# Kernel tuning notes

Measured on AMD Instinct MI355X. Metric: run time of the kernel, lower is better.

Reference implementation:

```python
import jax, jax.numpy as jnp
import numpy as np


def setup_inputs() -> dict:
    key = jax.random.key(0)
    k1, k2, k3, k4, k5 = jax.random.split(key, 5)
    B, T, H = 32, 4096, 256
    D = 2 * H  # encoder feature dim
    hidden = jax.random.normal(k1, (B, D), dtype=jnp.float32)
    encoder_outputs = jax.random.normal(k2, (B, T, D), dtype=jnp.float32)
    # torch nn.Linear(4H, H): weight [H, 4H], bias [H]
    W_attn = jax.random.normal(k3, (H, 4 * H), dtype=jnp.float32) * (1.0 / np.sqrt(4 * H))
    b_attn = jax.random.normal(k4, (H,), dtype=jnp.float32) * 0.01
    v = jax.random.uniform(k5, (H,), dtype=jnp.float32)  # torch.rand init
    return {"hidden": hidden, "encoder_outputs": encoder_outputs,
            "W_attn": W_attn, "b_attn": b_attn, "v": v}


def reference(hidden, encoder_outputs, W_attn, b_attn, v):
    D = hidden.shape[-1]  # 2*H
    # Split Linear(4H->H) weight into the hidden part and encoder part so we
    # never materialize the [B,T,4H] concat: cat(h,e) @ W.T == h @ Wh.T + e @ We.T
    W_h = W_attn[:, :D]   # [H, 2H]
    W_e = W_attn[:, D:]   # [H, 2H]
    h_proj = hidden @ W_h.T                     # [B, H]
    e_proj = jnp.einsum('btd,hd->bth', encoder_outputs, W_e)  # [B, T, H]
    energy = jnp.tanh(h_proj[:, None, :] + e_proj + b_attn)   # [B, T, H]
    scores = energy @ v                          # [B, T]
    attn_weights = jax.nn.softmax(scores, axis=1)  # softmax over timesteps
    context = jnp.einsum('bt,btd->bd', attn_weights, encoder_outputs)  # [B, 2H]
    return context, attn_weights
```

## Files before the change

kernel.cpp:

```cpp
#include <hip/hip_runtime.h>
#include <hip/hip_bf16.h>
#include <math.h>

#define B_  32
#define T_  4096
#define H_  256
#define D_  512

#define WS_PRE    0
#define WS_WEHI   32768
#define WS_P      294912
#define WS_ML     819200
#define WS_PCTX   827392

using short8  = __attribute__((ext_vector_type(8))) short;
using float4v = __attribute__((ext_vector_type(4))) float;

__device__ __forceinline__ unsigned cvt2_bf16(float lo, float hi) {
    union { __hip_bfloat162 h; unsigned u; } cv;
    cv.h = __float22bfloat162_rn(make_float2(lo, hi));
    return cv.u;
}
__device__ __forceinline__ short8 cvt8_bf16(const float* a) {
    union { unsigned u[4]; short8 s; } r;
    r.u[0] = cvt2_bf16(a[0], a[1]);
    r.u[1] = cvt2_bf16(a[2], a[3]);
    r.u[2] = cvt2_bf16(a[4], a[5]);
    r.u[3] = cvt2_bf16(a[6], a[7]);
    return r.s;
}

__device__ __forceinline__ float fast_tanh(float x) {
    float e = __expf(2.0f * x);
    return 1.0f - 2.0f * __builtin_amdgcn_rcpf(e + 1.0f);
}

__global__ __launch_bounds__(256)
void prep_kernel(const float* __restrict__ hidden,
                 const float* __restrict__ W_attn,
                 const float* __restrict__ b_attn,
                 unsigned char* __restrict__ ws) {
    int blk = blockIdx.x;
    int tid = threadIdx.x;
    if (blk < 32) {
        int b = blk, h = tid;
        const float4* hv = (const float4*)(hidden + b * D_);
        const float4* wv = (const float4*)(W_attn + (size_t)h * 1024);
        float s = 0.f;
        #pragma unroll 4
        for (int d4 = 0; d4 < D_ / 4; ++d4) {
            float4 a = hv[d4], w = wv[d4];
            s += a.x * w.x + a.y * w.y + a.z * w.z + a.w * w.w;
        }
        ((float*)(ws + WS_PRE))[b * H_ + h] = s + b_attn[h];
    } else {
        int q = (blk - 32) * 256 + tid;
        unsigned short* whi = (unsigned short*)(ws + WS_WEHI);
        #pragma unroll
        for (int i = 0; i < 4; ++i) {
            int idx4 = q + i * 8192;
            int n = idx4 >> 7, k = (idx4 & 127) << 2;
            int t = k >> 5, kin = k & 31;
            int quad = kin >> 3, e = kin & 7;
            int slot = quad ^ ((n >> 1) & 3);
            float4 w = *(const float4*)(W_attn + (size_t)n * 1024 + 512 + k);
            unsigned lo = cvt2_bf16(w.x, w.y);
            unsigned hi = cvt2_bf16(w.z, w.w);
            unsigned short* dst = whi + t * 8192 + n * 32 + slot * 8 + e;
            *(uint2*)dst = make_uint2(lo, hi);
        }
    }
}

#define BM 128
#define BN 256
#define BK 32
#define LDT 40
#define KIT 16

__global__ __launch_bounds__(512, 4)
void gemm_scores_kernel(const float* __restrict__ enc,
                        unsigned char* __restrict__ ws,
                        const float* __restrict__ v) {
    __shared__ unsigned short sA[2][BM * LDT];
    __shared__ float sScoreP[4][BM];
    __shared__ float sP[BM];
    __shared__ float sRed[4];

    const float*          pre = (const float*)(ws + WS_PRE);
    const unsigned short* weh = (const unsigned short*)(ws + WS_WEHI);

    int tid = threadIdx.x;
    int m0  = blockIdx.x * BM;
    int b   = m0 >> 12;

    int rowA = tid & 127, cgA = tid >> 7;
    const float* gA = enc + (size_t)(m0 + rowA) * D_ + cgA * 8;

    int wave = tid >> 6, lane = tid & 63;
    int wm = wave & 1, wn = wave >> 1;
    int quad = lane >> 4, l16 = lane & 15;

    int slotB = quad ^ ((l16 >> 1) & 3);
    const unsigned short* bBase = weh + (wn * 64 + l16) * 32 + slotB * 8;

    float4v acc[4][4] = {};

    float aX[8], aY[8];
    short8 bhA[4], bhB[4];

    {
        const float4* p0 = (const float4*)gA;
        float4 x0 = p0[0], x1 = p0[1];
        #pragma unroll
        for (int j = 0; j < 4; ++j)
            bhA[j] = *(const short8*)(bBase + j * 512);
        const float4* p1 = (const float4*)(gA + BK);
        float4 y0 = p1[0], y1 = p1[1];
        #pragma unroll
        for (int j = 0; j < 4; ++j)
            bhB[j] = *(const short8*)(bBase + 8192 + j * 512);

        float tmp[8];
        *(float4*)tmp = x0; *(float4*)(tmp + 4) = x1;
        *(short8*)&sA[0][rowA * LDT + cgA * 8] = cvt8_bf16(tmp);
        *(float4*)aY = y0; *(float4*)(aY + 4) = y1;
    }
    __builtin_amdgcn_s_waitcnt(0xc07f);
    __builtin_amdgcn_s_barrier();

#define K_STEP(kk, CUR, NXT, Acons, Aload, Bcur, Bnxt)                        \
    {                                                                         \
        if ((kk) + 1 < KIT) {                                                 \
            const unsigned short* pb = bBase + ((kk) + 1) * 8192;             \
            Bnxt[0] = *(const short8*)(pb);                                   \
            Bnxt[1] = *(const short8*)(pb + 512);                             \
            Bnxt[2] = *(const short8*)(pb + 1024);                            \
            Bnxt[3] = *(const short8*)(pb + 1536);                            \
        }                                                                     \
        if ((kk) + 2 < KIT) {                                                 \
            const float4* pa = (const float4*)(gA + ((kk) + 2) * BK);         \
            *(float4*)(Aload) = pa[0]; *(float4*)((Aload) + 4) = pa[1];       \
        }                                                                     \
        short8 ah[4];                                                         \
        _Pragma("unroll")                                                     \
        for (int i = 0; i < 4; ++i) {                                         \
            int r = wm * 64 + i * 16 + l16;                                   \
            ah[i] = *(const short8*)&sA[CUR][r * LDT + quad * 8];             \
        }                                                                     \
        _Pragma("unroll")                                                     \
        for (int i = 0; i < 4; ++i)                                           \
            _Pragma("unroll")                                                 \
            for (int j = 0; j < 4; ++j)                                       \
                acc[i][j] = __builtin_amdgcn_mfma_f32_16x16x32_bf16(          \
                    ah[i], Bcur[j], acc[i][j], 0, 0, 0);                      \
        if ((kk) + 1 < KIT) {                                                 \
            *(short8*)&sA[NXT][rowA * LDT + cgA * 8] = cvt8_bf16(Acons);      \
            __builtin_amdgcn_s_waitcnt(0xc07f);                               \
            __builtin_amdgcn_s_barrier();                                     \
        }                                                                     \
    }

    for (int kt = 0; kt < 8; ++kt) {
        K_STEP(2 * kt,     0, 1, aY, aX, bhA, bhB)
        K_STEP(2 * kt + 1, 1, 0, aX, aY, bhB, bhA)
    }
#undef K_STEP

    float rowsum[4][4] = {};
    #pragma unroll
    for (int j = 0; j < 4; ++j) {
        int n = wn * 64 + j * 16 + l16;
        float pv = pre[b * H_ + n];
        float vv = v[n];
        #pragma unroll
        for (int i = 0; i < 4; ++i)
            #pragma unroll
            for (int r = 0; r < 4; ++r)
                rowsum[i][r] += fast_tanh(acc[i][j][r] + pv) * vv;
    }
    #pragma unroll
    for (int i = 0; i < 4; ++i)
        #pragma unroll
        for (int r = 0; r < 4; ++r) {
            float s = rowsum[i][r];
            s += __shfl_xor(s, 1);
            s += __shfl_xor(s, 2);
            s += __shfl_xor(s, 4);
            s += __shfl_xor(s, 8);
            rowsum[i][r] = s;
        }
    if (l16 == 0) {
        #pragma unroll
        for (int i = 0; i < 4; ++i)
            #pragma unroll
            for (int r = 0; r < 4; ++r) {
                int row = wm * 64 + i * 16 + quad * 4 + r;
                sScoreP[wn][row] = rowsum[i][r];
            }
    }
    __syncthreads();

    float sval = 0.f;
    if (tid < 128) {
        sval = sScoreP[0][tid] + sScoreP[1][tid]
             + sScoreP[2][tid] + sScoreP[3][tid];
        float m = sval;
        #pragma unroll
        for (int off = 32; off; off >>= 1) m = fmaxf(m, __shfl_xor(m, off));
        if (lane == 0) sRed[wave] = m;
    }
    __syncthreads();
    float m_blk = fmaxf(sRed[0], sRed[1]);
    if (tid < 128) {
        float p = expf(sval - m_blk);
        sP[tid] = p;
        ((float*)(ws + WS_P))[m0 + tid] = p;
        float l = p;
        #pragma unroll
        for (int off = 32; off; off >>= 1) l += __shfl_xor(l, off);
        if (lane == 0) sRed[2 + wave] = l;
    }
    __syncthreads();
    if (tid == 0) {
        float2 ml = make_float2(m_blk, sRed[2] + sRed[3]);
        ((float2*)(ws + WS_ML))[blockIdx.x] = ml;
    }

    int colg = tid & 127, rgrp = tid >> 7;
    const float* encb = enc + (size_t)m0 * D_;
    float4 c4 = {0.f, 0.f, 0.f, 0.f};
    #pragma unroll 4
    for (int s = 0; s < 32; ++s) {
        int r = rgrp + 4 * s;
        float w = sP[r];
        float4 ev = *(const float4*)(encb + (size_t)r * D_ + colg * 4);
        c4.x += w * ev.x; c4.y += w * ev.y;
        c4.z += w * ev.z; c4.w += w * ev.w;
    }
    float4* red4 = (float4*)sA;
    red4[tid] = c4;
    __syncthreads();
    if (rgrp == 0) {
        float4 a0 = red4[colg], a1 = red4[colg + 128];
        float4 a2 = red4[colg + 256], a3 = red4[colg + 384];
        float4 o;
        o.x = a0.x + a1.x + a2.x + a3.x;
        o.y = a0.y + a1.y + a2.y + a3.y;
        o.z = a0.z + a1.z + a2.z + a3.z;
        o.w = a0.w + a1.w + a2.w + a3.w;
        ((float4*)(ws + WS_PCTX))[blockIdx.x * 128 + colg] = o;
    }
}

__global__ __launch_bounds__(512)
void finalize_kernel(const unsigned char* __restrict__ ws,
                     float* __restrict__ out_ctx,
                     float* __restrict__ out_w) {
    __shared__ float sm[32], sl[32], sscale[32];
    int b = blockIdx.x, tid = threadIdx.x;
    const float2* ml  = ((const float2*)(ws + WS_ML)) + b * 32;
    if (tid < 32) {
        float2 v = ml[tid];
        sm[tid] = v.x; sl[tid] = v.y;
    }
    __syncthreads();
    float m = -1e30f;
    #pragma unroll
    for (int i = 0; i < 32; ++i) m = fmaxf(m, sm[i]);
    float l = 0.f;
    #pragma unroll
    for (int i = 0; i < 32; ++i) l += sl[i] * expf(sm[i] - m);
    float inv = 1.0f / l;
    if (tid < 32) sscale[tid] = expf(sm[tid] - m) * inv;
    __syncthreads();

    {
        const float4* pb = (const float4*)((const float*)(ws + WS_P) + (size_t)b * T_);
        float4* wb = (float4*)(out_w + (size_t)b * T_);
        int t0 = tid * 2;
        float sc = sscale[tid >> 4];
        float4 x = pb[t0], y = pb[t0 + 1];
        x.x *= sc; x.y *= sc; x.z *= sc; x.w *= sc;
        y.x *= sc; y.y *= sc; y.z *= sc; y.w *= sc;
        wb[t0] = x; wb[t0 + 1] = y;
    }
    {
        const float* pc = (const float*)(ws + WS_PCTX) + (size_t)b * 32 * D_;
        float c = 0.f;
        #pragma unroll
        for (int i = 0; i < 32; ++i) c += pc[i * D_ + tid] * sscale[i];
        out_ctx[b * D_ + tid] = c;
    }
}

extern "C" void kernel_launch(void* const* d_in, const int* in_sizes, int n_in,
                              void* d_out, int out_size, void* d_ws, size_t ws_size,
                              hipStream_t stream) {
    const float* hidden = (const float*)d_in[0];
    const float* enc    = (const float*)d_in[1];
    const float* W_attn = (const float*)d_in[2];
    const float* b_attn = (const float*)d_in[3];
    const float* v      = (const float*)d_in[4];
    float* out = (float*)d_out;
    unsigned char* ws = (unsigned char*)d_ws;

    prep_kernel<<<64, 256, 0, stream>>>(hidden, W_attn, b_attn, ws);
    gemm_scores_kernel<<<T_ * B_ / BM, 512, 0, stream>>>(enc, ws, v);
    finalize_kernel<<<B_, 512, 0, stream>>>(ws, out, out + B_ * D_);
}
```

Before: 419.3 us.

## Fuse finalize into GEMM via last-block counter and process two tiles per block

The separate finalize kernel is removed. Each batch now keeps an atomic counter, and the last block to finish a batch performs the softmax rescale and the context reduction for it. The GEMM grid shrinks from 1024 to 512 blocks, and each block handles two tiles 512 apart, prefetching the second tile's first K-slices while the first tile's epilogue runs. This saves a kernel launch and overlaps part of the load latency, at the cost of threadfence/atomic overhead, a serial tail on the last block of each batch, and fewer blocks in flight.

```diff
diff --git a/kernel.cpp b/kernel.cpp
--- a/kernel.cpp
+++ b/kernel.cpp
@@ -12,6 +12,7 @@
 #define WS_P      294912
 #define WS_ML     819200
 #define WS_PCTX   827392
+#define WS_CNT    2924544
 
 using short8  = __attribute__((ext_vector_type(8))) short;
 using float4v = __attribute__((ext_vector_type(4))) float;
@@ -54,6 +55,7 @@
         }
         ((float*)(ws + WS_PRE))[b * H_ + h] = s + b_attn[h];
     } else {
+        if (blk == 32 && tid < 32) ((int*)(ws + WS_CNT))[tid] = 0;
         int q = (blk - 32) * 256 + tid;
         unsigned short* whi = (unsigned short*)(ws + WS_WEHI);
         #pragma unroll
@@ -81,22 +83,21 @@
 __global__ __launch_bounds__(512, 4)
 void gemm_scores_kernel(const float* __restrict__ enc,
                         unsigned char* __restrict__ ws,
-                        const float* __restrict__ v) {
+                        const float* __restrict__ v,
+                        float* __restrict__ out_ctx,
+                        float* __restrict__ out_w) {
     __shared__ unsigned short sA[2][BM * LDT];
     __shared__ float sScoreP[4][BM];
     __shared__ float sP[BM];
     __shared__ float sRed[4];
-
-    const float*          pre = (const float*)(ws + WS_PRE);
-    const unsigned short* weh = (const unsigned short*)(ws + WS_WEHI);
+    __shared__ int   sLastFlag;
+
+    const float*          pre_all = (const float*)(ws + WS_PRE);
+    const unsigned short* weh     = (const unsigned short*)(ws + WS_WEHI);
+    int*                  cnt     = (int*)(ws + WS_CNT);
 
     int tid = threadIdx.x;
-    int m0  = blockIdx.x * BM;
-    int b   = m0 >> 12;
-
     int rowA = tid & 127, cgA = tid >> 7;
-    const float* gA = enc + (size_t)(m0 + rowA) * D_ + cgA * 8;
-
     int wave = tid >> 6, lane = tid & 63;
     int wm = wave & 1, wn = wave >> 1;
     int quad = lane >> 4, l16 = lane & 15;
@@ -104,30 +105,34 @@
     int slotB = quad ^ ((l16 >> 1) & 3);
     const unsigned short* bBase = weh + (wn * 64 + l16) * 32 + slotB * 8;
 
-    float4v acc[4][4] = {};
-
     float aX[8], aY[8];
     short8 bhA[4], bhB[4];
 
+    int tile = blockIdx.x;
+    int finBatch[2] = {-1, -1};
+
     {
-        const float4* p0 = (const float4*)gA;
-        float4 x0 = p0[0], x1 = p0[1];
-        #pragma unroll
-        for (int j = 0; j < 4; ++j)
-            bhA[j] = *(const short8*)(bBase + j * 512);
-        const float4* p1 = (const float4*)(gA + BK);
-        float4 y0 = p1[0], y1 = p1[1];
-        #pragma unroll
-        for (int j = 0; j < 4; ++j)
-            bhB[j] = *(const short8*)(bBase + 8192 + j * 512);
-
-        float tmp[8];
-        *(float4*)tmp = x0; *(float4*)(tmp + 4) = x1;
-        *(short8*)&sA[0][rowA * LDT + cgA * 8] = cvt8_bf16(tmp);
-        *(float4*)aY = y0; *(float4*)(aY + 4) = y1;
-    }
-    __builtin_amdgcn_s_waitcnt(0xc07f);
-    __builtin_amdgcn_s_barrier();
+        const float* gA0 = enc + (size_t)(tile * BM + rowA) * D_ + cgA * 8;
+        const float4* p0 = (const float4*)gA0;
+        *(float4*)aX = p0[0]; *(float4*)(aX + 4) = p0[1];
+        #pragma unroll
+        for (int j = 0; j < 4; ++j) bhA[j] = *(const short8*)(bBase + j * 512);
+        const float4* p1 = (const float4*)(gA0 + BK);
+        *(float4*)aY = p1[0]; *(float4*)(aY + 4) = p1[1];
+        #pragma unroll
+        for (int j = 0; j < 4; ++j) bhB[j] = *(const short8*)(bBase + 8192 + j * 512);
+    }
+
+    for (int tt = 0; tt < 2; ++tt) {
+        int m0 = tile * BM;
+        int b  = m0 >> 12;
+        const float* gA = enc + (size_t)(m0 + rowA) * D_ + cgA * 8;
+
+        *(short8*)&sA[0][rowA * LDT + cgA * 8] = cvt8_bf16(aX);
+        __builtin_amdgcn_s_waitcnt(0xc07f);
+        __builtin_amdgcn_s_barrier();
+
+        float4v acc[4][4] = {};
 
 #define K_STEP(kk, CUR, NXT, Acons, Aload, Bcur, Bnxt)                        \
     {                                                                         \
@@ -161,136 +166,159 @@
         }                                                                     \
     }
 
-    for (int kt = 0; kt < 8; ++kt) {
-        K_STEP(2 * kt,     0, 1, aY, aX, bhA, bhB)
-        K_STEP(2 * kt + 1, 1, 0, aX, aY, bhB, bhA)
-    }
+        for (int kt = 0; kt < 8; ++kt) {
+            K_STEP(2 * kt,     0, 1, aY, aX, bhA, bhB)
+            K_STEP(2 * kt + 1, 1, 0, aX, aY, bhB, bhA)
+        }
 #undef K_STEP
 
-    float rowsum[4][4] = {};
+        float rowsum[4][4] = {};
+        #pragma unroll
+        for (int j = 0; j < 4; ++j) {
+            int n = wn * 64 + j * 16 + l16;
+            float pv = pre_all[b * H_ + n];
+            float vv = v[n];
+            #pragma unroll
+            for (int i = 0; i < 4; ++i)
+                #pragma unroll
+                for (int r = 0; r < 4; ++r)
+                    rowsum[i][r] += fast_tanh(acc[i][j][r] + pv) * vv;
+        }
+        #pragma unroll
+        for (int i = 0; i < 4; ++i)
+            #pragma unroll
+            for (int r = 0; r < 4; ++r) {
+                float s = rowsum[i][r];
+                s += __shfl_xor(s, 1);
+                s += __shfl_xor(s, 2);
+                s += __shfl_xor(s, 4);
+                s += __shfl_xor(s, 8);
+                rowsum[i][r] = s;
+            }
+        if (l16 == 0) {
+            #pragma unroll
+            for (int i = 0; i < 4; ++i)
+                #pragma unroll
+                for (int r = 0; r < 4; ++r) {
+                    int row = wm * 64 + i * 16 + quad * 4 + r;
+                    sScoreP[wn][row] = rowsum[i][r];
+                }
+        }
+        __syncthreads();
+
+        if (tt == 0) {
+            const float* gAn = enc + (size_t)((tile + 512) * BM + rowA) * D_ + cgA * 8;
+            const float4* p0 = (const float4*)gAn;
+            *(float4*)aX = p0[0]; *(float4*)(aX + 4) = p0[1];
+            #pragma unroll
+            for (int j = 0; j < 4; ++j) bhA[j] = *(const short8*)(bBase + j * 512);
+            const float4* p1 = (const float4*)(gAn + BK);
+            *(float4*)aY = p1[0]; *(float4*)(aY + 4) = p1[1];
+            #pragma unroll
+            for (int j = 0; j < 4; ++j) bhB[j] = *(const short8*)(bBase + 8192 + j * 512);
+        }
+
+        float sval = 0.f;
+        if (tid < 128) {
+            sval = sScoreP[0][tid] + sScoreP[1][tid]
+                 + sScoreP[2][tid] + sScoreP[3][tid];
+            float m = sval;
+            #pragma unroll
+            for (int off = 32; off; off >>= 1) m = fmaxf(m, __shfl_xor(m, off));
+            if (lane == 0) sRed[wave] = m;
+        }
+        __syncthreads();
+        float m_blk = fmaxf(sRed[0], sRed[1]);
+        if (tid < 128) {
+            float p = expf(sval - m_blk);
+            sP[tid] = p;
+            ((float*)(ws + WS_P))[m0 + tid] = p;
+            float l = p;
+            #pragma unroll
+            for (int off = 32; off; off >>= 1) l += __shfl_xor(l, off);
+            if (lane == 0) sRed[2 + wave] = l;
+        }
+        __syncthreads();
+        if (tid == 0) {
+            float2 ml = make_float2(m_blk, sRed[2] + sRed[3]);
+            ((float2*)(ws + WS_ML))[tile] = ml;
+        }
+
+        int colg = tid & 127, rgrp = tid >> 7;
+        const float* encb = enc + (size_t)m0 * D_;
+        float4 c4 = {0.f, 0.f, 0.f, 0.f};
+        #pragma unroll 4
+        for (int s = 0; s < 32; ++s) {
+            int r = rgrp + 4 * s;
+            float w = sP[r];
+            float4 ev = *(const float4*)(encb + (size_t)r * D_ + colg * 4);
+            c4.x += w * ev.x; c4.y += w * ev.y;
+            c4.z += w * ev.z; c4.w += w * ev.w;
+        }
+        float4* red4 = (float4*)sA;
+        red4[tid] = c4;
+        __syncthreads();
+        if (rgrp == 0) {
+            float4 a0 = red4[colg], a1 = red4[colg + 128];
+            float4 a2 = red4[colg + 256], a3 = red4[colg + 384];
+            float4 o;
+            o.x = a0.x + a1.x + a2.x + a3.x;
+            o.y = a0.y + a1.y + a2.y + a3.y;
+            o.z = a0.z + a1.z + a2.z + a3.z;
+            o.w = a0.w + a1.w + a2.w + a3.w;
+            ((float4*)(ws + WS_PCTX))[tile * 128 + colg] = o;
+        }
+
+        __threadfence();
+        __syncthreads();
+        if (tid == 0) sLastFlag = (atomicAdd(&cnt[b], 1) == 31);
+        __syncthreads();
+        if (sLastFlag) finBatch[tt] = b;
+
+        tile += 512;
+    }
+
     #pragma unroll
-    for (int j = 0; j < 4; ++j) {
-        int n = wn * 64 + j * 16 + l16;
-        float pv = pre[b * H_ + n];
-        float vv = v[n];
-        #pragma unroll
-        for (int i = 0; i < 4; ++i)
-            #pragma unroll
-            for (int r = 0; r < 4; ++r)
-                rowsum[i][r] += fast_tanh(acc[i][j][r] + pv) * vv;
-    }
-    #pragma unroll
-    for (int i = 0; i < 4; ++i)
-        #pragma unroll
-        for (int r = 0; r < 4; ++r) {
-            float s = rowsum[i][r];
-            s += __shfl_xor(s, 1);
-            s += __shfl_xor(s, 2);
-            s += __shfl_xor(s, 4);
-            s += __shfl_xor(s, 8);
-            rowsum[i][r] = s;
-        }
-    if (l16 == 0) {
-        #pragma unroll
-        for (int i = 0; i < 4; ++i)
-            #pragma unroll
-            for (int r = 0; r < 4; ++r) {
-                int row = wm * 64 + i * 16 + quad * 4 + r;
-                sScoreP[wn][row] = rowsum[i][r];
-            }
-    }
-    __syncthreads();
-
-    float sval = 0.f;
-    if (tid < 128) {
-        sval = sScoreP[0][tid] + sScoreP[1][tid]
-             + sScoreP[2][tid] + sScoreP[3][tid];
-        float m = sval;
-        #pragma unroll
-        for (int off = 32; off; off >>= 1) m = fmaxf(m, __shfl_xor(m, off));
-        if (lane == 0) sRed[wave] = m;
-    }
-    __syncthreads();
-    float m_blk = fmaxf(sRed[0], sRed[1]);
-    if (tid < 128) {
-        float p = expf(sval - m_blk);
-        sP[tid] = p;
-        ((float*)(ws + WS_P))[m0 + tid] = p;
-        float l = p;
-        #pragma unroll
-        for (int off = 32; off; off >>= 1) l += __shfl_xor(l, off);
-        if (lane == 0) sRed[2 + wave] = l;
-    }
-    __syncthreads();
-    if (tid == 0) {
-        float2 ml = make_float2(m_blk, sRed[2] + sRed[3]);
-        ((float2*)(ws + WS_ML))[blockIdx.x] = ml;
-    }
-
-    int colg = tid & 127, rgrp = tid >> 7;
-    const float* encb = enc + (size_t)m0 * D_;
-    float4 c4 = {0.f, 0.f, 0.f, 0.f};
-    #pragma unroll 4
-    for (int s = 0; s < 32; ++s) {
-        int r = rgrp + 4 * s;
-        float w = sP[r];
-        float4 ev = *(const float4*)(encb + (size_t)r * D_ + colg * 4);
-        c4.x += w * ev.x; c4.y += w * ev.y;
-        c4.z += w * ev.z; c4.w += w * ev.w;
-    }
-    float4* red4 = (float4*)sA;
-    red4[tid] = c4;
-    __syncthreads();
-    if (rgrp == 0) {
-        float4 a0 = red4[colg], a1 = red4[colg + 128];
-        float4 a2 = red4[colg + 256], a3 = red4[colg + 384];
-        float4 o;
-        o.x = a0.x + a1.x + a2.x + a3.x;
-        o.y = a0.y + a1.y + a2.y + a3.y;
-        o.z = a0.z + a1.z + a2.z + a3.z;
-        o.w = a0.w + a1.w + a2.w + a3.w;
-        ((float4*)(ws + WS_PCTX))[blockIdx.x * 128 + colg] = o;
-    }
-}
-
-__global__ __launch_bounds__(512)
-void finalize_kernel(const unsigned char* __restrict__ ws,
-                     float* __restrict__ out_ctx,
-                     float* __restrict__ out_w) {
-    __shared__ float sm[32], sl[32], sscale[32];
-    int b = blockIdx.x, tid = threadIdx.x;
-    const float2* ml  = ((const float2*)(ws + WS_ML)) + b * 32;
-    if (tid < 32) {
-        float2 v = ml[tid];
-        sm[tid] = v.x; sl[tid] = v.y;
-    }
-    __syncthreads();
-    float m = -1e30f;
-    #pragma unroll
-    for (int i = 0; i < 32; ++i) m = fmaxf(m, sm[i]);
-    float l = 0.f;
-    #pragma unroll
-    for (int i = 0; i < 32; ++i) l += sl[i] * expf(sm[i] - m);
-    float inv = 1.0f / l;
-    if (tid < 32) sscale[tid] = expf(sm[tid] - m) * inv;
-    __syncthreads();
-
-    {
-        const float4* pb = (const float4*)((const float*)(ws + WS_P) + (size_t)b * T_);
-        float4* wb = (float4*)(out_w + (size_t)b * T_);
-        int t0 = tid * 2;
-        float sc = sscale[tid >> 4];
-        float4 x = pb[t0], y = pb[t0 + 1];
-        x.x *= sc; x.y *= sc; x.z *= sc; x.w *= sc;
-        y.x *= sc; y.y *= sc; y.z *= sc; y.w *= sc;
-        wb[t0] = x; wb[t0 + 1] = y;
-    }
-    {
-        const float* pc = (const float*)(ws + WS_PCTX) + (size_t)b * 32 * D_;
-        float c = 0.f;
-        #pragma unroll
-        for (int i = 0; i < 32; ++i) c += pc[i * D_ + tid] * sscale[i];
-        out_ctx[b * D_ + tid] = c;
+    for (int q = 0; q < 2; ++q) {
+        int fb = finBatch[q];
+        if (fb < 0) continue;
+        __threadfence();
+        float* sm     = &sScoreP[0][0];
+        float* sl     = &sScoreP[0][32];
+        float* sscale = &sScoreP[0][64];
+        __syncthreads();
+        const float2* mlp = ((const float2*)(ws + WS_ML)) + fb * 32;
+        if (tid < 32) {
+            float2 vml = mlp[tid];
+            sm[tid] = vml.x; sl[tid] = vml.y;
+        }
+        __syncthreads();
+        float m = -1e30f;
+        #pragma unroll
+        for (int i = 0; i < 32; ++i) m = fmaxf(m, sm[i]);
+        float l = 0.f;
+        #pragma unroll
+        for (int i = 0; i < 32; ++i) l += sl[i] * expf(sm[i] - m);
+        float inv = 1.0f / l;
+        if (tid < 32) sscale[tid] = expf(sm[tid] - m) * inv;
+        __syncthreads();
+        {
+            const float4* pb = (const float4*)((const float*)(ws + WS_P) + (size_t)fb * T_);
+            float4* wb = (float4*)(out_w + (size_t)fb * T_);
+            int t0 = tid * 2;
+            float sc = sscale[tid >> 4];
+            float4 x = pb[t0], y = pb[t0 + 1];
+            x.x *= sc; x.y *= sc; x.z *= sc; x.w *= sc;
+            y.x *= sc; y.y *= sc; y.z *= sc; y.w *= sc;
+            wb[t0] = x; wb[t0 + 1] = y;
+        }
+        {
+            const float* pc = (const float*)(ws + WS_PCTX) + (size_t)fb * 32 * D_;
+            float c = 0.f;
+            #pragma unroll
+            for (int i = 0; i < 32; ++i) c += pc[i * D_ + tid] * sscale[i];
+            out_ctx[fb * D_ + tid] = c;
+        }
     }
 }
 
@@ -306,6 +334,5 @@
     unsigned char* ws = (unsigned char*)d_ws;
 
     prep_kernel<<<64, 256, 0, stream>>>(hidden, W_attn, b_attn, ws);
-    gemm_scores_kernel<<<T_ * B_ / BM, 512, 0, stream>>>(enc, ws, v);
-    finalize_kernel<<<B_, 512, 0, stream>>>(ws, out, out + B_ * D_);
-}
+    gemm_scores_kernel<<<512, 512, 0, stream>>>(enc, ws, v, out, out + B_ * D_);
+}
```

Result: slower. 914.0 us (+118.0%).

## Keep full bf16 encoder tile in LDS and reuse it for context

Applied to the files above, without the earlier changes.

The kernel now keeps the whole 128x512 encoder tile in shared memory as bf16 instead of double-buffering one 32-column slice. The context accumulation reads from that LDS copy, so it no longer re-reads the fp32 encoder rows from global memory. The cost is about 130KB of LDS per block, which drops occupancy (launch bounds go from 4 to 2). The context sum is also now computed from bf16-rounded encoder values rather than fp32, which loses precision.

```diff
diff --git a/kernel.cpp b/kernel.cpp
--- a/kernel.cpp
+++ b/kernel.cpp
@@ -28,6 +28,11 @@
     r.u[2] = cvt2_bf16(a[4], a[5]);
     r.u[3] = cvt2_bf16(a[6], a[7]);
     return r.s;
+}
+
+__device__ __forceinline__ float bf16_to_f32(unsigned short u) {
+    unsigned v = ((unsigned)u) << 16;
+    return __uint_as_float(v);
 }
 
 __device__ __forceinline__ float fast_tanh(float x) {
@@ -75,14 +80,14 @@
 #define BM 128
 #define BN 256
 #define BK 32
-#define LDT 40
+#define LDT 520
 #define KIT 16
 
-__global__ __launch_bounds__(512, 4)
+__global__ __launch_bounds__(512, 2)
 void gemm_scores_kernel(const float* __restrict__ enc,
                         unsigned char* __restrict__ ws,
                         const float* __restrict__ v) {
-    __shared__ unsigned short sA[2][BM * LDT];
+    __shared__ unsigned short sE[BM * LDT];
     __shared__ float sScoreP[4][BM];
     __shared__ float sP[BM];
     __shared__ float sRed[4];
@@ -123,13 +128,13 @@
 
         float tmp[8];
         *(float4*)tmp = x0; *(float4*)(tmp + 4) = x1;
-        *(short8*)&sA[0][rowA * LDT + cgA * 8] = cvt8_bf16(tmp);
+        *(short8*)&sE[rowA * LDT + cgA * 8] = cvt8_bf16(tmp);
         *(float4*)aY = y0; *(float4*)(aY + 4) = y1;
     }
     __builtin_amdgcn_s_waitcnt(0xc07f);
     __builtin_amdgcn_s_barrier();
 
-#define K_STEP(kk, CUR, NXT, Acons, Aload, Bcur, Bnxt)                        \
+#define K_STEP(kk, Acons, Aload, Bcur, Bnxt)                                  \
     {                                                                         \
         if ((kk) + 1 < KIT) {                                                 \
             const unsigned short* pb = bBase + ((kk) + 1) * 8192;             \
@@ -146,7 +151,7 @@
         _Pragma("unroll")                                                     \
         for (int i = 0; i < 4; ++i) {                                         \
             int r = wm * 64 + i * 16 + l16;                                   \
-            ah[i] = *(const short8*)&sA[CUR][r * LDT + quad * 8];             \
+            ah[i] = *(const short8*)&sE[r * LDT + (kk) * BK + quad * 8];      \
         }                                                                     \
         _Pragma("unroll")                                                     \
         for (int i = 0; i < 4; ++i)                                           \
@@ -155,15 +160,16 @@
                 acc[i][j] = __builtin_amdgcn_mfma_f32_16x16x32_bf16(          \
                     ah[i], Bcur[j], acc[i][j], 0, 0, 0);                      \
         if ((kk) + 1 < KIT) {                                                 \
-            *(short8*)&sA[NXT][rowA * LDT + cgA * 8] = cvt8_bf16(Acons);      \
+            *(short8*)&sE[rowA * LDT + ((kk) + 1) * BK + cgA * 8] =           \
+                cvt8_bf16(Acons);                                             \
             __builtin_amdgcn_s_waitcnt(0xc07f);                               \
             __builtin_amdgcn_s_barrier();                                     \
         }                                                                     \
     }
 
     for (int kt = 0; kt < 8; ++kt) {
-        K_STEP(2 * kt,     0, 1, aY, aX, bhA, bhB)
-        K_STEP(2 * kt + 1, 1, 0, aX, aY, bhB, bhA)
+        K_STEP(2 * kt,     aY, aX, bhA, bhB)
+        K_STEP(2 * kt + 1, aX, aY, bhB, bhA)
     }
 #undef K_STEP
 
@@ -228,17 +234,19 @@
     }
 
     int colg = tid & 127, rgrp = tid >> 7;
-    const float* encb = enc + (size_t)m0 * D_;
     float4 c4 = {0.f, 0.f, 0.f, 0.f};
     #pragma unroll 4
     for (int s = 0; s < 32; ++s) {
         int r = rgrp + 4 * s;
         float w = sP[r];
-        float4 ev = *(const float4*)(encb + (size_t)r * D_ + colg * 4);
-        c4.x += w * ev.x; c4.y += w * ev.y;
-        c4.z += w * ev.z; c4.w += w * ev.w;
-    }
-    float4* red4 = (float4*)sA;
+        uint2 raw = *(const uint2*)&sE[r * LDT + colg * 4];
+        c4.x += w * bf16_to_f32((unsigned short)(raw.x & 0xffffu));
+        c4.y += w * bf16_to_f32((unsigned short)(raw.x >> 16));
+        c4.z += w * bf16_to_f32((unsigned short)(raw.y & 0xffffu));
+        c4.w += w * bf16_to_f32((unsigned short)(raw.y >> 16));
+    }
+    __syncthreads();
+    float4* red4 = (float4*)sE;
     red4[tid] = c4;
     __syncthreads();
     if (rgrp == 0) {
```

Result: no change. 421.2 us (+0.4%).
